# Kernel optimization log

Measured on AMD Instinct MI355X. Metric: run time of the kernel, lower is better.

The kernel has to match this reference:

```python
import jax, jax.numpy as jnp
import numpy as np

H = 1024      # hidden_size
L = 128       # max_length
V = 50257     # output_size (vocab)


def setup_inputs() -> dict:
    key = jax.random.key(0)
    ks = jax.random.split(key, 16)
    s = 1.0 / np.sqrt(H)
    inp = {
        "x": jax.random.randint(ks[0], (1,), 0, V, dtype=jnp.int64)
        if jax.config.jax_enable_x64 else jax.random.randint(ks[0], (1,), 0, V, dtype=jnp.int32),
        "hidden": jax.random.normal(ks[1], (1, 1, H), dtype=jnp.float32),
        "encoder_outputs": jax.random.normal(ks[2], (L, H), dtype=jnp.float32),
        # learned parameters
        "emb": jax.random.normal(ks[3], (V, H), dtype=jnp.float32),
        "attn_W": jax.random.uniform(ks[4], (L, 2 * H), jnp.float32, -s, s),
        "attn_b": jax.random.uniform(ks[5], (L,), jnp.float32, -s, s),
        "comb_W": jax.random.uniform(ks[6], (H, 2 * H), jnp.float32, -s, s),
        "comb_b": jax.random.uniform(ks[7], (H,), jnp.float32, -s, s),
        "W_ih": jax.random.uniform(ks[8], (3 * H, H), jnp.float32, -s, s),
        "W_hh": jax.random.uniform(ks[9], (3 * H, H), jnp.float32, -s, s),
        "b_ih": jax.random.uniform(ks[10], (3 * H,), jnp.float32, -s, s),
        "b_hh": jax.random.uniform(ks[11], (3 * H,), jnp.float32, -s, s),
        "out_W": jax.random.uniform(ks[12], (V, H), jnp.float32, -s, s),
        "out_b": jax.random.uniform(ks[13], (V,), jnp.float32, -s, s),
    }
    return inp


def _gru_cell(x_t, h, W_ih, W_hh, b_ih, b_hh):
    # PyTorch GRU gate order: r, z, n
    gx = x_t @ W_ih.T + b_ih              # [1, 3H]
    gh = h @ W_hh.T + b_hh                # [1, 3H]
    gx_r, gx_z, gx_n = jnp.split(gx, 3, axis=1)
    gh_r, gh_z, gh_n = jnp.split(gh, 3, axis=1)
    r = jax.nn.sigmoid(gx_r + gh_r)
    z = jax.nn.sigmoid(gx_z + gh_z)
    n = jnp.tanh(gx_n + r * gh_n)
    return (1.0 - z) * n + z * h          # [1, H]


def reference(x, hidden, encoder_outputs, emb, attn_W, attn_b, comb_W, comb_b,
              W_ih, W_hh, b_ih, b_hh, out_W, out_b):
    embedded = emb[x]                                        # [1, H]
    h0 = hidden[0]                                           # [1, H]
    cat_eh = jnp.concatenate([embedded, h0], axis=1)         # [1, 2H]
    attention_weights = jax.nn.softmax(cat_eh @ attn_W.T + attn_b, axis=1)  # [1, L]
    with_attention = attention_weights @ encoder_outputs     # [1, H]
    combined = jnp.concatenate([embedded, with_attention], axis=1)  # [1, 2H]
    rnn_in = jax.nn.relu(combined @ comb_W.T + comb_b)       # [1, H]
    h_new = _gru_cell(rnn_in, h0, W_ih, W_hh, b_ih, b_hh)    # [1, H]
    logp = jax.nn.log_softmax(h_new @ out_W.T + out_b, axis=1)  # [1, V]
    return logp, h_new[None, :, :], attention_weights
```

## Files before the change

### kernel.cpp

```cpp
#include <hip/hip_runtime.h>
#include <math.h>

#define H 1024
#define L 128
#define V 50257
#define NB6 2048

#define WS_AL    0
#define WS_WATT  128
#define WS_RNN   (128+1024)
#define WS_GX    (128+2048)
#define WS_GH    (128+2048+3072)
#define WS_PM    (128+2048+6144)
#define WS_PS    (WS_PM + NB6)

__device__ __forceinline__ float wred(float v) {
    v += __shfl_down(v, 32);
    v += __shfl_down(v, 16);
    v += __shfl_down(v, 8);
    v += __shfl_down(v, 4);
    v += __shfl_down(v, 2);
    v += __shfl_down(v, 1);
    return v;
}

__global__ __launch_bounds__(256) void k_attn_gh(
        const float* __restrict__ emb, const int* __restrict__ x,
        const float* __restrict__ hid, const float* __restrict__ attn_W,
        const float* __restrict__ attn_b, const float* __restrict__ W_hh,
        const float* __restrict__ b_hh, float* __restrict__ ws) {
    int w = blockIdx.x * 4 + (threadIdx.x >> 6);
    int lane = threadIdx.x & 63;
    if (w < L) {
        const float* er = emb + (size_t)x[0] * H;
        const float* aw = attn_W + (size_t)w * (2 * H);
        float acc = 0.f;
        #pragma unroll
        for (int k = 0; k < 8; ++k) {
            int j = (k * 64 + lane) * 4;
            float4 wv = *(const float4*)(aw + j);
            const float* src = (j < H) ? (er + j) : (hid + (j - H));
            float4 cv = *(const float4*)src;
            acc += wv.x * cv.x + wv.y * cv.y + wv.z * cv.z + wv.w * cv.w;
        }
        acc = wred(acc);
        if (lane == 0) ws[WS_AL + w] = acc + attn_b[w];
    } else {
        int r = w - L;
        const float* wr = W_hh + (size_t)r * H;
        float acc = 0.f;
        #pragma unroll
        for (int k = 0; k < 4; ++k) {
            int j = (k * 64 + lane) * 4;
            float4 wv = *(const float4*)(wr + j);
            float4 hv = *(const float4*)(hid + j);
            acc += wv.x * hv.x + wv.y * hv.y + wv.z * hv.z + wv.w * hv.w;
        }
        acc = wred(acc);
        if (lane == 0) ws[WS_GH + r] = acc + b_hh[r];
    }
}

__global__ __launch_bounds__(256) void k_attn_apply(
        const float* __restrict__ enc, float* __restrict__ ws,
        float* __restrict__ out) {
    __shared__ float sl[L];
    __shared__ float swt[L];
    __shared__ float part[4][64];
    int t = threadIdx.x;
    if (t < L) sl[t] = ws[WS_AL + t];
    __syncthreads();
    float m = -1e30f;
    #pragma unroll 8
    for (int i = 0; i < L; ++i) m = fmaxf(m, sl[i]);
    float s = 0.f;
    #pragma unroll 4
    for (int i = 0; i < L; ++i) s += expf(sl[i] - m);
    float inv = 1.f / s;
    if (t < L) swt[t] = expf(sl[t] - m) * inv;
    __syncthreads();
    int col = t & 63, q = t >> 6;
    int h = blockIdx.x * 64 + col;
    float acc = 0.f;
    #pragma unroll 8
    for (int l = q * 32; l < q * 32 + 32; ++l) acc += swt[l] * enc[l * H + h];
    part[q][col] = acc;
    __syncthreads();
    if (q == 0)
        ws[WS_WATT + h] = part[0][col] + part[1][col] + part[2][col] + part[3][col];
    if (blockIdx.x == 0 && t < L) out[V + H + t] = swt[t];
}

__global__ __launch_bounds__(256) void k_rnn_in(
        const float* __restrict__ emb, const int* __restrict__ x,
        const float* __restrict__ comb_W, const float* __restrict__ comb_b,
        float* __restrict__ ws) {
    int wave = blockIdx.x * 4 + (threadIdx.x >> 6);
    int lane = threadIdx.x & 63;
    const float* er = emb + (size_t)x[0] * H;
    const float* w  = comb_W + (size_t)wave * (2 * H);
    const float* watt = ws + WS_WATT;
    float acc = 0.f;
    #pragma unroll
    for (int k = 0; k < 8; ++k) {
        int j = (k * 64 + lane) * 4;
        float4 wv = *(const float4*)(w + j);
        const float* src = (j < H) ? (er + j) : (watt + (j - H));
        float4 cv = *(const float4*)src;
        acc += wv.x * cv.x + wv.y * cv.y + wv.z * cv.z + wv.w * cv.w;
    }
    acc = wred(acc);
    if (lane == 0) ws[WS_RNN + wave] = fmaxf(acc + comb_b[wave], 0.f);
}

__global__ __launch_bounds__(256) void k_gx(
        const float* __restrict__ W_ih, const float* __restrict__ b_ih,
        float* __restrict__ ws) {
    int r = blockIdx.x * 4 + (threadIdx.x >> 6);
    int lane = threadIdx.x & 63;
    const float* w = W_ih + (size_t)r * H;
    const float* rn = ws + WS_RNN;
    float acc = 0.f;
    #pragma unroll
    for (int k = 0; k < 4; ++k) {
        int j = (k * 64 + lane) * 4;
        float4 wv = *(const float4*)(w + j);
        float4 rv = *(const float4*)(rn + j);
        acc += wv.x * rv.x + wv.y * rv.y + wv.z * rv.z + wv.w * rv.w;
    }
    acc = wred(acc);
    if (lane == 0) ws[WS_GX + r] = acc + b_ih[r];
}

__global__ __launch_bounds__(256) void k_logits(
        const float* __restrict__ out_W, const float* __restrict__ out_b,
        const float* __restrict__ hid, float* __restrict__ ws,
        float* __restrict__ out) {
    __shared__ float sh[H];
    int t = threadIdx.x;
    const float* gx = ws + WS_GX;
    const float* gh = ws + WS_GH;
    #pragma unroll
    for (int i = t; i < H; i += 256) {
        float r = 1.f / (1.f + expf(-(gx[i] + gh[i])));
        float z = 1.f / (1.f + expf(-(gx[H + i] + gh[H + i])));
        float n = tanhf(gx[2 * H + i] + r * gh[2 * H + i]);
        float hn = (1.f - z) * n + z * hid[i];
        sh[i] = hn;
        if (blockIdx.x == 0) out[V + i] = hn;
    }
    __syncthreads();

    int wid = t >> 6;
    int lane = t & 63;
    int gw = blockIdx.x * 4 + wid;
    float m = -INFINITY, s = 0.f;
    for (int row = gw; row < V; row += NB6 * 4) {
        const float* w = out_W + (size_t)row * H;
        float acc = 0.f;
        #pragma unroll
        for (int k = 0; k < 4; ++k) {
            int j = (k * 64 + lane) * 4;
            float4 wv = *(const float4*)(w + j);
            float4 hv = *(const float4*)(sh + j);
            acc += wv.x * hv.x + wv.y * hv.y + wv.z * hv.z + wv.w * hv.w;
        }
        acc = wred(acc);
        if (lane == 0) {
            float logit = acc + out_b[row];
            out[row] = logit;
            if (logit > m) { s = s * expf(m - logit) + 1.f; m = logit; }
            else           { s += expf(logit - m); }
        }
    }
    __shared__ float sm[4], ss[4];
    if (lane == 0) { sm[wid] = m; ss[wid] = s; }
    __syncthreads();
    if (t == 0) {
        float M = fmaxf(fmaxf(sm[0], sm[1]), fmaxf(sm[2], sm[3]));
        float S = ss[0] * expf(sm[0] - M) + ss[1] * expf(sm[1] - M)
                + ss[2] * expf(sm[2] - M) + ss[3] * expf(sm[3] - M);
        ws[WS_PM + blockIdx.x] = M;
        ws[WS_PS + blockIdx.x] = S;
    }
}

__global__ __launch_bounds__(256) void k_finalize(
        float* __restrict__ out, const float* __restrict__ ws) {
    __shared__ float sm[256], ss[256];
    int t = threadIdx.x;
    float m = -INFINITY, s = 0.f;
    for (int i = t; i < NB6; i += 256) {
        float mi = ws[WS_PM + i], si = ws[WS_PS + i];
        float M = fmaxf(m, mi);
        s = s * expf(m - M) + si * expf(mi - M);
        m = M;
    }
    sm[t] = m; ss[t] = s;
    __syncthreads();
    for (int off = 128; off > 0; off >>= 1) {
        if (t < off) {
            float m2 = sm[t + off], s2 = ss[t + off];
            float M = fmaxf(sm[t], m2);
            ss[t] = ss[t] * expf(sm[t] - M) + s2 * expf(m2 - M);
            sm[t] = M;
        }
        __syncthreads();
    }
    float lse = sm[0] + logf(ss[0]);
    int i = blockIdx.x * 256 + t;
    if (i < V) out[i] -= lse;
}

extern "C" void kernel_launch(void* const* d_in, const int* in_sizes, int n_in,
                              void* d_out, int out_size, void* d_ws, size_t ws_size,
                              hipStream_t stream) {
    const int*   x      = (const int*)  d_in[0];
    const float* hidden = (const float*)d_in[1];
    const float* enc    = (const float*)d_in[2];
    const float* emb    = (const float*)d_in[3];
    const float* attn_W = (const float*)d_in[4];
    const float* attn_b = (const float*)d_in[5];
    const float* comb_W = (const float*)d_in[6];
    const float* comb_b = (const float*)d_in[7];
    const float* W_ih   = (const float*)d_in[8];
    const float* W_hh   = (const float*)d_in[9];
    const float* b_ih   = (const float*)d_in[10];
    const float* b_hh   = (const float*)d_in[11];
    const float* out_W  = (const float*)d_in[12];
    const float* out_b  = (const float*)d_in[13];
    float* out = (float*)d_out;
    float* ws  = (float*)d_ws;

    k_attn_gh    <<<800, 256, 0, stream>>>(emb, x, hidden, attn_W, attn_b, W_hh, b_hh, ws);
    k_attn_apply <<<16, 256, 0, stream>>>(enc, ws, out);
    k_rnn_in     <<<256, 256, 0, stream>>>(emb, x, comb_W, comb_b, ws);
    k_gx         <<<768, 256, 0, stream>>>(W_ih, b_ih, ws);
    k_logits     <<<NB6, 256, 0, stream>>>(out_W, out_b, hidden, ws, out);
    k_finalize   <<<(V + 255) / 256, 256, 0, stream>>>(out, ws);
}
```

Before: 432.6 us.

## Fuse all decoder stages into one cooperative persistent kernel with grid syncs

Replaces six separate kernel launches with a single cooperative kernel that walks through the attention, combine, GRU, logits and log-softmax stages, separated by grid-wide barriers. Grid size is taken from the occupancy query and capped at 1792 blocks. The aim is to remove per-launch overhead and inter-kernel gaps. In exchange it adds five grid.sync barriers, and small stages such as attention apply run on only 16 blocks while the rest of the grid waits.

Result: slower. 803.5 us (+85.7%).

```diff
diff --git a/kernel.cpp b/kernel.cpp
--- a/kernel.cpp
+++ b/kernel.cpp
@@ -1,10 +1,12 @@
 #include <hip/hip_runtime.h>
+#include <hip/hip_cooperative_groups.h>
 #include <math.h>
+
+namespace cg = cooperative_groups;
 
 #define H 1024
 #define L 128
 #define V 50257
-#define NB6 2048
 
 #define WS_AL    0
 #define WS_WATT  128
@@ -12,7 +14,7 @@
 #define WS_GX    (128+2048)
 #define WS_GH    (128+2048+3072)
 #define WS_PM    (128+2048+6144)
-#define WS_PS    (WS_PM + NB6)
+#define WS_PS    (WS_PM + 2048)
 
 __device__ __forceinline__ float wred(float v) {
     v += __shfl_down(v, 32);
@@ -24,192 +26,187 @@
     return v;
 }
 
-__global__ __launch_bounds__(256) void k_attn_gh(
-        const float* __restrict__ emb, const int* __restrict__ x,
-        const float* __restrict__ hid, const float* __restrict__ attn_W,
-        const float* __restrict__ attn_b, const float* __restrict__ W_hh,
-        const float* __restrict__ b_hh, float* __restrict__ ws) {
-    int w = blockIdx.x * 4 + (threadIdx.x >> 6);
-    int lane = threadIdx.x & 63;
-    if (w < L) {
-        const float* er = emb + (size_t)x[0] * H;
-        const float* aw = attn_W + (size_t)w * (2 * H);
+__global__ __launch_bounds__(256, 7) void k_fused(
+        const int* __restrict__ x, const float* __restrict__ hid,
+        const float* __restrict__ enc, const float* __restrict__ emb,
+        const float* __restrict__ attn_W, const float* __restrict__ attn_b,
+        const float* __restrict__ comb_W, const float* __restrict__ comb_b,
+        const float* __restrict__ W_ih, const float* __restrict__ W_hh,
+        const float* __restrict__ b_ih, const float* __restrict__ b_hh,
+        const float* __restrict__ out_W, const float* __restrict__ out_b,
+        float* __restrict__ ws, float* __restrict__ out) {
+    cg::grid_group grid = cg::this_grid();
+    __shared__ float sA[H];
+    __shared__ float sB[512];
+
+    const int t    = threadIdx.x;
+    const int lane = t & 63;
+    const int wid  = t >> 6;
+    const int nb   = gridDim.x;
+    const int nw   = nb * 4;
+    const int gw   = blockIdx.x * 4 + wid;
+    const float* er = emb + (size_t)x[0] * H;
+
+    for (int w = gw; w < L + 3 * H; w += nw) {
+        if (w < L) {
+            const float* aw = attn_W + (size_t)w * (2 * H);
+            float acc = 0.f;
+            #pragma unroll
+            for (int k = 0; k < 8; ++k) {
+                int j = (k * 64 + lane) * 4;
+                float4 wv = *(const float4*)(aw + j);
+                const float* src = (j < H) ? (er + j) : (hid + (j - H));
+                float4 cv = *(const float4*)src;
+                acc += wv.x * cv.x + wv.y * cv.y + wv.z * cv.z + wv.w * cv.w;
+            }
+            acc = wred(acc);
+            if (lane == 0) ws[WS_AL + w] = acc + attn_b[w];
+        } else {
+            int r = w - L;
+            const float* wr = W_hh + (size_t)r * H;
+            float acc = 0.f;
+            #pragma unroll
+            for (int k = 0; k < 4; ++k) {
+                int j = (k * 64 + lane) * 4;
+                float4 wv = *(const float4*)(wr + j);
+                float4 hv = *(const float4*)(hid + j);
+                acc += wv.x * hv.x + wv.y * hv.y + wv.z * hv.z + wv.w * hv.w;
+            }
+            acc = wred(acc);
+            if (lane == 0) ws[WS_GH + r] = acc + b_hh[r];
+        }
+    }
+    grid.sync();
+
+    {
+        if (t < L) sA[t] = ws[WS_AL + t];
+        __syncthreads();
+        float m = -1e30f;
+        #pragma unroll 8
+        for (int i = 0; i < L; ++i) m = fmaxf(m, sA[i]);
+        float s = 0.f;
+        #pragma unroll 4
+        for (int i = 0; i < L; ++i) s += expf(sA[i] - m);
+        float inv = 1.f / s;
+        if (t < L) sA[L + t] = expf(sA[t] - m) * inv;
+        __syncthreads();
+        if (blockIdx.x == 0 && t < L) out[V + H + t] = sA[L + t];
+        int col = t & 63, q = t >> 6;
+        for (int g = blockIdx.x; g < 16; g += nb) {
+            int h = g * 64 + col;
+            float acc = 0.f;
+            #pragma unroll 8
+            for (int l = q * 32; l < q * 32 + 32; ++l)
+                acc += sA[L + l] * enc[l * H + h];
+            sB[q * 64 + col] = acc;
+            __syncthreads();
+            if (q == 0)
+                ws[WS_WATT + h] = sB[col] + sB[64 + col] + sB[128 + col] + sB[192 + col];
+            __syncthreads();
+        }
+    }
+    grid.sync();
+
+    for (int row = gw; row < H; row += nw) {
+        const float* w = comb_W + (size_t)row * (2 * H);
+        const float* watt = ws + WS_WATT;
         float acc = 0.f;
         #pragma unroll
         for (int k = 0; k < 8; ++k) {
             int j = (k * 64 + lane) * 4;
-            float4 wv = *(const float4*)(aw + j);
-            const float* src = (j < H) ? (er + j) : (hid + (j - H));
+            float4 wv = *(const float4*)(w + j);
+            const float* src = (j < H) ? (er + j) : (watt + (j - H));
             float4 cv = *(const float4*)src;
             acc += wv.x * cv.x + wv.y * cv.y + wv.z * cv.z + wv.w * cv.w;
         }
         acc = wred(acc);
-        if (lane == 0) ws[WS_AL + w] = acc + attn_b[w];
-    } else {
-        int r = w - L;
-        const float* wr = W_hh + (size_t)r * H;
-        float acc = 0.f;
-        #pragma unroll
-        for (int k = 0; k < 4; ++k) {
-            int j = (k * 64 + lane) * 4;
-            float4 wv = *(const float4*)(wr + j);
-            float4 hv = *(const float4*)(hid + j);
-            acc += wv.x * hv.x + wv.y * hv.y + wv.z * hv.z + wv.w * hv.w;
-        }
-        acc = wred(acc);
-        if (lane == 0) ws[WS_GH + r] = acc + b_hh[r];
-    }
-}
-
-__global__ __launch_bounds__(256) void k_attn_apply(
-        const float* __restrict__ enc, float* __restrict__ ws,
-        float* __restrict__ out) {
-    __shared__ float sl[L];
-    __shared__ float swt[L];
-    __shared__ float part[4][64];
-    int t = threadIdx.x;
-    if (t < L) sl[t] = ws[WS_AL + t];
-    __syncthreads();
-    float m = -1e30f;
-    #pragma unroll 8
-    for (int i = 0; i < L; ++i) m = fmaxf(m, sl[i]);
-    float s = 0.f;
-    #pragma unroll 4
-    for (int i = 0; i < L; ++i) s += expf(sl[i] - m);
-    float inv = 1.f / s;
-    if (t < L) swt[t] = expf(sl[t] - m) * inv;
-    __syncthreads();
-    int col = t & 63, q = t >> 6;
-    int h = blockIdx.x * 64 + col;
-    float acc = 0.f;
-    #pragma unroll 8
-    for (int l = q * 32; l < q * 32 + 32; ++l) acc += swt[l] * enc[l * H + h];
-    part[q][col] = acc;
-    __syncthreads();
-    if (q == 0)
-        ws[WS_WATT + h] = part[0][col] + part[1][col] + part[2][col] + part[3][col];
-    if (blockIdx.x == 0 && t < L) out[V + H + t] = swt[t];
-}
-
-__global__ __launch_bounds__(256) void k_rnn_in(
-        const float* __restrict__ emb, const int* __restrict__ x,
-        const float* __restrict__ comb_W, const float* __restrict__ comb_b,
-        float* __restrict__ ws) {
-    int wave = blockIdx.x * 4 + (threadIdx.x >> 6);
-    int lane = threadIdx.x & 63;
-    const float* er = emb + (size_t)x[0] * H;
-    const float* w  = comb_W + (size_t)wave * (2 * H);
-    const float* watt = ws + WS_WATT;
-    float acc = 0.f;
-    #pragma unroll
-    for (int k = 0; k < 8; ++k) {
-        int j = (k * 64 + lane) * 4;
-        float4 wv = *(const float4*)(w + j);
-        const float* src = (j < H) ? (er + j) : (watt + (j - H));
-        float4 cv = *(const float4*)src;
-        acc += wv.x * cv.x + wv.y * cv.y + wv.z * cv.z + wv.w * cv.w;
-    }
-    acc = wred(acc);
-    if (lane == 0) ws[WS_RNN + wave] = fmaxf(acc + comb_b[wave], 0.f);
-}
-
-__global__ __launch_bounds__(256) void k_gx(
-        const float* __restrict__ W_ih, const float* __restrict__ b_ih,
-        float* __restrict__ ws) {
-    int r = blockIdx.x * 4 + (threadIdx.x >> 6);
-    int lane = threadIdx.x & 63;
-    const float* w = W_ih + (size_t)r * H;
-    const float* rn = ws + WS_RNN;
-    float acc = 0.f;
-    #pragma unroll
-    for (int k = 0; k < 4; ++k) {
-        int j = (k * 64 + lane) * 4;
-        float4 wv = *(const float4*)(w + j);
-        float4 rv = *(const float4*)(rn + j);
-        acc += wv.x * rv.x + wv.y * rv.y + wv.z * rv.z + wv.w * rv.w;
-    }
-    acc = wred(acc);
-    if (lane == 0) ws[WS_GX + r] = acc + b_ih[r];
-}
-
-__global__ __launch_bounds__(256) void k_logits(
-        const float* __restrict__ out_W, const float* __restrict__ out_b,
-        const float* __restrict__ hid, float* __restrict__ ws,
-        float* __restrict__ out) {
-    __shared__ float sh[H];
-    int t = threadIdx.x;
-    const float* gx = ws + WS_GX;
-    const float* gh = ws + WS_GH;
-    #pragma unroll
-    for (int i = t; i < H; i += 256) {
-        float r = 1.f / (1.f + expf(-(gx[i] + gh[i])));
-        float z = 1.f / (1.f + expf(-(gx[H + i] + gh[H + i])));
-        float n = tanhf(gx[2 * H + i] + r * gh[2 * H + i]);
-        float hn = (1.f - z) * n + z * hid[i];
-        sh[i] = hn;
-        if (blockIdx.x == 0) out[V + i] = hn;
-    }
-    __syncthreads();
-
-    int wid = t >> 6;
-    int lane = t & 63;
-    int gw = blockIdx.x * 4 + wid;
-    float m = -INFINITY, s = 0.f;
-    for (int row = gw; row < V; row += NB6 * 4) {
-        const float* w = out_W + (size_t)row * H;
+        if (lane == 0) ws[WS_RNN + row] = fmaxf(acc + comb_b[row], 0.f);
+    }
+    grid.sync();
+
+    for (int r = gw; r < 3 * H; r += nw) {
+        const float* w = W_ih + (size_t)r * H;
+        const float* rn = ws + WS_RNN;
         float acc = 0.f;
         #pragma unroll
         for (int k = 0; k < 4; ++k) {
             int j = (k * 64 + lane) * 4;
             float4 wv = *(const float4*)(w + j);
-            float4 hv = *(const float4*)(sh + j);
-            acc += wv.x * hv.x + wv.y * hv.y + wv.z * hv.z + wv.w * hv.w;
+            float4 rv = *(const float4*)(rn + j);
+            acc += wv.x * rv.x + wv.y * rv.y + wv.z * rv.z + wv.w * rv.w;
         }
         acc = wred(acc);
-        if (lane == 0) {
-            float logit = acc + out_b[row];
-            out[row] = logit;
-            if (logit > m) { s = s * expf(m - logit) + 1.f; m = logit; }
-            else           { s += expf(logit - m); }
-        }
-    }
-    __shared__ float sm[4], ss[4];
-    if (lane == 0) { sm[wid] = m; ss[wid] = s; }
-    __syncthreads();
-    if (t == 0) {
-        float M = fmaxf(fmaxf(sm[0], sm[1]), fmaxf(sm[2], sm[3]));
-        float S = ss[0] * expf(sm[0] - M) + ss[1] * expf(sm[1] - M)
-                + ss[2] * expf(sm[2] - M) + ss[3] * expf(sm[3] - M);
-        ws[WS_PM + blockIdx.x] = M;
-        ws[WS_PS + blockIdx.x] = S;
-    }
-}
-
-__global__ __launch_bounds__(256) void k_finalize(
-        float* __restrict__ out, const float* __restrict__ ws) {
-    __shared__ float sm[256], ss[256];
-    int t = threadIdx.x;
-    float m = -INFINITY, s = 0.f;
-    for (int i = t; i < NB6; i += 256) {
-        float mi = ws[WS_PM + i], si = ws[WS_PS + i];
-        float M = fmaxf(m, mi);
-        s = s * expf(m - M) + si * expf(mi - M);
-        m = M;
-    }
-    sm[t] = m; ss[t] = s;
-    __syncthreads();
-    for (int off = 128; off > 0; off >>= 1) {
-        if (t < off) {
-            float m2 = sm[t + off], s2 = ss[t + off];
-            float M = fmaxf(sm[t], m2);
-            ss[t] = ss[t] * expf(sm[t] - M) + s2 * expf(m2 - M);
-            sm[t] = M;
-        }
-        __syncthreads();
-    }
-    float lse = sm[0] + logf(ss[0]);
-    int i = blockIdx.x * 256 + t;
-    if (i < V) out[i] -= lse;
+        if (lane == 0) ws[WS_GX + r] = acc + b_ih[r];
+    }
+    grid.sync();
+
+    {
+        const float* gx = ws + WS_GX;
+        const float* gh = ws + WS_GH;
+        #pragma unroll
+        for (int i = t; i < H; i += 256) {
+            float r = 1.f / (1.f + expf(-(gx[i] + gh[i])));
+            float z = 1.f / (1.f + expf(-(gx[H + i] + gh[H + i])));
+            float n = tanhf(gx[2 * H + i] + r * gh[2 * H + i]);
+            float hn = (1.f - z) * n + z * hid[i];
+            sA[i] = hn;
+            if (blockIdx.x == 0) out[V + i] = hn;
+        }
+        __syncthreads();
+        float m = -INFINITY, s = 0.f;
+        for (int row = gw; row < V; row += nw) {
+            const float* w = out_W + (size_t)row * H;
+            float acc = 0.f;
+            #pragma unroll
+            for (int k = 0; k < 4; ++k) {
+                int j = (k * 64 + lane) * 4;
+                float4 wv = *(const float4*)(w + j);
+                float4 hv = *(const float4*)(sA + j);
+                acc += wv.x * hv.x + wv.y * hv.y + wv.z * hv.z + wv.w * hv.w;
+            }
+            acc = wred(acc);
+            if (lane == 0) {
+                float logit = acc + out_b[row];
+                out[row] = logit;
+                if (logit > m) { s = s * expf(m - logit) + 1.f; m = logit; }
+                else           { s += expf(logit - m); }
+            }
+        }
+        if (lane == 0) { sB[wid] = m; sB[4 + wid] = s; }
+        __syncthreads();
+        if (t == 0) {
+            float M = fmaxf(fmaxf(sB[0], sB[1]), fmaxf(sB[2], sB[3]));
+            float S = sB[4] * expf(sB[0] - M) + sB[5] * expf(sB[1] - M)
+                    + sB[6] * expf(sB[2] - M) + sB[7] * expf(sB[3] - M);
+            ws[WS_PM + blockIdx.x] = M;
+            ws[WS_PS + blockIdx.x] = S;
+        }
+    }
+    grid.sync();
+
+    {
+        float m = -INFINITY, s = 0.f;
+        for (int i = t; i < nb; i += 256) {
+            float mi = ws[WS_PM + i], si = ws[WS_PS + i];
+            float M = fmaxf(m, mi);
+            s = s * expf(m - M) + si * expf(mi - M);
+            m = M;
+        }
+        sB[t] = m; sB[256 + t] = s;
+        __syncthreads();
+        for (int off = 128; off > 0; off >>= 1) {
+            if (t < off) {
+                float m2 = sB[t + off], s2 = sB[256 + t + off];
+                float M = fmaxf(sB[t], m2);
+                sB[256 + t] = sB[256 + t] * expf(sB[t] - M) + s2 * expf(m2 - M);
+                sB[t] = M;
+            }
+            __syncthreads();
+        }
+        float lse = sB[0] + logf(sB[256]);
+        for (int i = blockIdx.x * 256 + t; i < V; i += nb * 256)
+            out[i] -= lse;
+    }
 }
 
 extern "C" void kernel_launch(void* const* d_in, const int* in_sizes, int n_in,
@@ -232,10 +229,16 @@
     float* out = (float*)d_out;
     float* ws  = (float*)d_ws;
 
-    k_attn_gh    <<<800, 256, 0, stream>>>(emb, x, hidden, attn_W, attn_b, W_hh, b_hh, ws);
-    k_attn_apply <<<16, 256, 0, stream>>>(enc, ws, out);
-    k_rnn_in     <<<256, 256, 0, stream>>>(emb, x, comb_W, comb_b, ws);
-    k_gx         <<<768, 256, 0, stream>>>(W_ih, b_ih, ws);
-    k_logits     <<<NB6, 256, 0, stream>>>(out_W, out_b, hidden, ws, out);
-    k_finalize   <<<(V + 255) / 256, 256, 0, stream>>>(out, ws);
+    int maxb = 0;
+    if (hipOccupancyMaxActiveBlocksPerMultiprocessor(&maxb, k_fused, 256, 0)
+            != hipSuccess || maxb < 1)
+        maxb = 4;
+    int nb = maxb * 256;
+    if (nb > 1792) nb = 1792;
+
+    void* args[] = {(void*)&x, (void*)&hidden, (void*)&enc, (void*)&emb,
+                    (void*)&attn_W, (void*)&attn_b, (void*)&comb_W, (void*)&comb_b,
+                    (void*)&W_ih, (void*)&W_hh, (void*)&b_ih, (void*)&b_hh,
+                    (void*)&out_W, (void*)&out_b, (void*)&ws, (void*)&out};
+    hipLaunchCooperativeKernel((void*)k_fused, dim3(nb), dim3(256), args, 0, stream);
 }
```
